# Kernel tuning notes

Hardware: AMD Instinct MI355X
Metric: run time of the kernel (lower is better)

The kernel has to match this reference:

```python
import jax, jax.numpy as jnp
import numpy as np

H, D = 16, 64  # head_num, head_dim
SCALE = 1.0 / D ** 0.5


def setup_inputs() -> dict:
    key = jax.random.key(0)
    ks = jax.random.split(key, 12)
    S, T, B, E = 2048, 2048, 2, 1024  # dec_seq, enc_seq, bs, input_dim
    return {
        "inputs": jax.random.normal(ks[0], (S, B, E), jnp.float32),
        "pos_embedding": jax.random.normal(ks[1], (T, 1, E), jnp.float32),
        "encoder_hidden_states": jax.random.normal(ks[2], (T, B, E), jnp.float32),
        "u": jax.random.normal(ks[3], (H, D), jnp.float32) * 0.02,
        "v": jax.random.normal(ks[4], (H, D), jnp.float32) * 0.02,
        "mask": jnp.zeros((S, T, 1), jnp.bool_),
        "Wkv": jax.random.normal(ks[5], (E, 2 * H * D), jnp.float32) * (E ** -0.5),
        "bkv": jnp.zeros((2 * H * D,), jnp.float32),
        "Wq": jax.random.normal(ks[6], (E, H * D), jnp.float32) * (E ** -0.5),
        "bq": jnp.zeros((H * D,), jnp.float32),
        "Wp": jax.random.normal(ks[7], (H * D, E), jnp.float32) * ((H * D) ** -0.5),
        "bp": jnp.zeros((E,), jnp.float32),
    }


def reference(inputs, pos_embedding, encoder_hidden_states, u, v, mask,
              Wkv, bkv, Wq, bq, Wp, bp):
    S, B, E = inputs.shape
    T = encoder_hidden_states.shape[0]
    # projections (fc_block == Linear)
    kv = encoder_hidden_states @ Wkv + bkv            # (T, B, 2HD)
    k, val = jnp.split(kv, 2, axis=-1)
    k = k.reshape(T, B, H, D)
    val = val.reshape(T, B, H, D)
    q = (inputs @ Wq + bq).reshape(S, B, H, D)
    q_u = q + u                                       # content bias (H, D) broadcast
    # content attention: (B, H, S, T)
    attn = jnp.einsum('sbhd,tbhd->bhst', q_u, k) * SCALE
    # mask (S, T, 1) -> (1, 1, S, T); all-False mask == original skip branch
    m = jnp.transpose(mask, (2, 0, 1))[:, None]
    attn = jnp.where(m, -jnp.inf, attn)
    attn = jax.nn.softmax(attn, axis=-1)
    # dropout is identity (eval)
    attn_vec = jnp.einsum('bhst,tbhd->sbhd', attn, val).reshape(S, B, H * D)
    return attn_vec @ Wp + bp                         # (S, B, E)
```

## Files before the change

### kernel.cpp

```cpp
#include <hip/hip_runtime.h>

#define Hh 16
#define Dd 64
#define Ss 2048
#define Tt 2048
#define Bb 2
#define Ee 1024
#define HD 1024
#define QSCALE 0.18033688011112042f

typedef __attribute__((ext_vector_type(8))) __bf16 bf16x8;
typedef __attribute__((ext_vector_type(4))) float f32x4;
typedef __attribute__((ext_vector_type(8))) unsigned short ushort8;

static __device__ __forceinline__ unsigned short f2b(float x) {
    union { float f; unsigned u; } v; v.f = x;
    unsigned r = v.u + 0x7FFFu + ((v.u >> 16) & 1u);
    return (unsigned short)(r >> 16);
}

static __device__ __forceinline__ unsigned cvtpk(float a, float b) {
    unsigned r;
    __asm__("v_cvt_pk_bf16_f32 %0, %1, %2" : "=v"(r) : "v"(a), "v"(b));
    return r;
}

static __device__ __forceinline__ void gld16(const unsigned short* g, unsigned short* l) {
    __builtin_amdgcn_global_load_lds(
        (const __attribute__((address_space(1))) unsigned int*)g,
        (__attribute__((address_space(3))) unsigned int*)l, 16, 0, 0);
}

__global__ __launch_bounds__(256) void prep(
    const float* __restrict__ enc, const float* __restrict__ inp,
    unsigned short* __restrict__ encb, unsigned short* __restrict__ inpb,
    const float* __restrict__ Wkv, const float* __restrict__ Wq, const float* __restrict__ Wp,
    unsigned short* __restrict__ Wkvt, unsigned short* __restrict__ Wqt,
    unsigned short* __restrict__ Wpt)
{
    __shared__ float tile[64][65];
    const int bx = blockIdx.x;
    const int tid = threadIdx.x;
    if (bx < 8192) {
        const int n4each = (Tt * Bb * Ee) / 4;
        int i = bx * 256 + tid;
        const float4* src; ushort4* dst; int j;
        if (i < n4each) { src = (const float4*)enc; dst = (ushort4*)encb; j = i; }
        else            { src = (const float4*)inp; dst = (ushort4*)inpb; j = i - n4each; }
        float4 v = src[j];
        ushort4 o; o.x = f2b(v.x); o.y = f2b(v.y); o.z = f2b(v.z); o.w = f2b(v.w);
        dst[j] = o;
        return;
    }
    int u = bx - 8192;
    const float* in; unsigned short* out; int C, cblk, rblk;
    if (u < 512)       { in = Wkv; out = Wkvt; C = 2048; cblk = u & 31; rblk = u >> 5; }
    else if (u < 768)  { int v = u - 512; in = Wq; out = Wqt; C = 1024; cblk = v & 15; rblk = v >> 4; }
    else               { int v = u - 768; in = Wp; out = Wpt; C = 1024; cblk = v & 15; rblk = v >> 4; }
    const int R = 1024;
    int c0 = cblk * 64, r0 = rblk * 64;
    int tx = tid & 63, ty = tid >> 6;
    for (int i = ty; i < 64; i += 4)
        tile[i][tx] = in[(r0 + i) * (long)C + c0 + tx];
    __syncthreads();
    int c_local = tid >> 2, g = tid & 3;
    ushort8 o0, o1;
#pragma unroll
    for (int k = 0; k < 8; k++) o0[k] = f2b(tile[g * 16 + k][c_local]);
#pragma unroll
    for (int k = 0; k < 8; k++) o1[k] = f2b(tile[g * 16 + 8 + k][c_local]);
    unsigned short* dst = &out[(c0 + c_local) * (long)R + r0 + g * 16];
    *(ushort8*)dst = o0;
    *(ushort8*)(dst + 8) = o1;
}

static __device__ __forceinline__ void gemm_core(
    const unsigned short* __restrict__ A, const unsigned short* __restrict__ Bt,
    int m0, int n0, unsigned short* lA, unsigned short* lB, f32x4 acc[4][4])
{
    const int tid = threadIdx.x;
    const int lane = tid & 63;
    const int wid = tid >> 6;
    const int waveM = (wid & 1) * 64, waveN = (wid >> 1) * 64;
    const int quad = lane >> 4, low = lane & 15;
#pragma unroll
    for (int i = 0; i < 4; i++)
#pragma unroll
        for (int j = 0; j < 4; j++) acc[i][j] = (f32x4)0.0f;

    for (int k0 = 0; k0 < 1024; k0 += 32) {
        __syncthreads();
        {
            int r0 = tid >> 2, s0 = tid & 3;
            int f1 = tid + 256, r1 = f1 >> 2, s1 = f1 & 3;
            gld16(&A[(m0 + r0) * 1024 + k0 + s0 * 8], &lA[tid * 8]);
            gld16(&A[(m0 + r1) * 1024 + k0 + s1 * 8], &lA[f1 * 8]);
            gld16(&Bt[(n0 + r0) * 1024 + k0 + s0 * 8], &lB[tid * 8]);
            gld16(&Bt[(n0 + r1) * 1024 + k0 + s1 * 8], &lB[f1 * 8]);
        }
        __syncthreads();
        bf16x8 af[4], bfr[4];
#pragma unroll
        for (int i = 0; i < 4; i++)
            af[i] = *(const bf16x8*)&lA[(waveM + i * 16 + low) * 32 + quad * 8];
#pragma unroll
        for (int j = 0; j < 4; j++)
            bfr[j] = *(const bf16x8*)&lB[(waveN + j * 16 + low) * 32 + quad * 8];
#pragma unroll
        for (int i = 0; i < 4; i++)
#pragma unroll
            for (int j = 0; j < 4; j++)
                acc[i][j] = __builtin_amdgcn_mfma_f32_16x16x32_bf16(af[i], bfr[j], acc[i][j], 0, 0, 0);
    }
}

__global__ __launch_bounds__(256) void gemm12(
    const unsigned short* __restrict__ encb, const unsigned short* __restrict__ Wkvt,
    const float* __restrict__ bkv,
    const unsigned short* __restrict__ inpb, const unsigned short* __restrict__ Wqt,
    const float* __restrict__ bq, const float* __restrict__ u,
    unsigned short* __restrict__ Kw, unsigned short* __restrict__ Vb,
    unsigned short* __restrict__ qw)
{
    __shared__ unsigned short smem[128 * 130];
    unsigned short* lA = smem;
    unsigned short* lB = smem + 128 * 32;
    const int bx = blockIdx.x;
    int z, m0, n0;
    const unsigned short *Ap, *Bp;
    if (bx < 512) { z = 0; m0 = (bx >> 4) * 128; n0 = (bx & 15) * 128; Ap = encb; Bp = Wkvt; }
    else { z = 1; int i = bx - 512; m0 = (i >> 3) * 128; n0 = (i & 7) * 128; Ap = inpb; Bp = Wqt; }
    f32x4 acc[4][4];
    gemm_core(Ap, Bp, m0, n0, lA, lB, acc);
    __syncthreads();

    const int lane = threadIdx.x & 63;
    const int wid = threadIdx.x >> 6;
    const int waveM = (wid & 1) * 64, waveN = (wid >> 1) * 64;
    const int quad = lane >> 4, low = lane & 15;
#pragma unroll
    for (int i = 0; i < 4; i++)
#pragma unroll
        for (int j = 0; j < 4; j++)
#pragma unroll
            for (int r = 0; r < 4; r++) {
                int lm = waveM + i * 16 + quad * 4 + r;
                int ln = waveN + j * 16 + low;
                int gn = n0 + ln;
                float val = acc[i][j][r];
                if (z == 0) val += bkv[gn];
                else        val = (val + bq[gn] + u[gn]) * QSCALE;
                smem[lm * 130 + ln] = f2b(val);
            }
    __syncthreads();

    const int tid = threadIdx.x;
    if (z == 0 && n0 >= 1024) {
        int d = tid & 63, hp = (tid >> 6) & 1, b = tid >> 7;
        int h = ((n0 - 1024) >> 6) + hp;
        int tb = m0 >> 7;
        unsigned short* dst = &Vb[((((b << 4) | h) * 32 + tb) * 64 + d) * 64];
#pragma unroll
        for (int c = 0; c < 8; c++) {
            ushort8 o;
#pragma unroll
            for (int k = 0; k < 8; k++)
                o[k] = smem[((c * 8 + k) * 2 + b) * 130 + hp * 64 + d];
            *(ushort8*)(dst + c * 8) = o;
        }
    } else {
        int gl = tid & 127, hp = tid >> 7;
        int gm = m0 + gl;
        int t = gm >> 1, b = gm & 1;
        int h = (n0 >> 6) + hp;
        unsigned short* base = (z == 0) ? Kw : qw;
        unsigned short* dst = &base[(((b << 4) | h) * 2048 + t) * 64];
        const unsigned short* src = &smem[gl * 130 + hp * 64];
#pragma unroll
        for (int c = 0; c < 8; c++) {
            ushort8 o;
#pragma unroll
            for (int k = 0; k < 8; k++) o[k] = src[c * 8 + k];
            *(ushort8*)(dst + c * 8) = o;
        }
    }
}

__global__ __launch_bounds__(256) void gemm3(
    const unsigned short* __restrict__ av, const unsigned short* __restrict__ Wpt,
    const float* __restrict__ bp, float* __restrict__ out)
{
    __shared__ unsigned short lA[128 * 32];
    __shared__ unsigned short lB[64 * 32];
    const int tid = threadIdx.x;
    const int lane = tid & 63;
    const int wid = tid >> 6;
    const int waveM = (wid & 1) * 64, waveN = (wid >> 1) * 32;
    const int m0 = blockIdx.y * 128, n0 = blockIdx.x * 64;
    const int quad = lane >> 4, low = lane & 15;

    f32x4 acc[4][2];
#pragma unroll
    for (int i = 0; i < 4; i++)
#pragma unroll
        for (int j = 0; j < 2; j++) acc[i][j] = (f32x4)0.0f;

    for (int k0 = 0; k0 < 1024; k0 += 32) {
        __syncthreads();
        {
            int r0 = tid >> 2, s0 = tid & 3;
            int f1 = tid + 256, r1 = f1 >> 2, s1 = f1 & 3;
            gld16(&av[(m0 + r0) * 1024 + k0 + s0 * 8], &lA[tid * 8]);
            gld16(&av[(m0 + r1) * 1024 + k0 + s1 * 8], &lA[f1 * 8]);
            gld16(&Wpt[(n0 + r0) * 1024 + k0 + s0 * 8], &lB[tid * 8]);
        }
        __syncthreads();
        bf16x8 af[4], bfr[2];
#pragma unroll
        for (int i = 0; i < 4; i++)
            af[i] = *(const bf16x8*)&lA[(waveM + i * 16 + low) * 32 + quad * 8];
#pragma unroll
        for (int j = 0; j < 2; j++)
            bfr[j] = *(const bf16x8*)&lB[(waveN + j * 16 + low) * 32 + quad * 8];
#pragma unroll
        for (int i = 0; i < 4; i++)
#pragma unroll
            for (int j = 0; j < 2; j++)
                acc[i][j] = __builtin_amdgcn_mfma_f32_16x16x32_bf16(af[i], bfr[j], acc[i][j], 0, 0, 0);
    }
#pragma unroll
    for (int i = 0; i < 4; i++)
#pragma unroll
        for (int j = 0; j < 2; j++)
#pragma unroll
            for (int r = 0; r < 4; r++) {
                int gm = m0 + waveM + i * 16 + quad * 4 + r;
                int gn = n0 + waveN + j * 16 + low;
                out[gm * 1024 + gn] = acc[i][j][r] + bp[gn];
            }
}

__global__ __launch_bounds__(256) void attn_kernel(
    const unsigned short* __restrict__ qw, const unsigned short* __restrict__ Kw,
    const unsigned short* __restrict__ Vb, unsigned short* __restrict__ av)
{
    __shared__ unsigned short kl[2][128 * 64];
    __shared__ unsigned short vt[2][64 * 64];
    __shared__ unsigned short pl[8][16 * 64];
    const int tid = threadIdx.x;
    const int lane = tid & 63;
    const int w = tid >> 6;
    const int quad = lane >> 4, low = lane & 15;
    const int swz = low & 7;
    const int bh = blockIdx.x & 31;
    const int s0 = (blockIdx.x >> 5) * 64;
    const int s_wave = s0 + w * 16;

    bf16x8 qf0, qf1;
    {
        const unsigned short* qa = &qw[(bh * 2048 + s_wave + low) * 64];
        qf0 = *(const bf16x8*)&qa[quad * 8];
        qf1 = *(const bf16x8*)&qa[32 + quad * 8];
    }
    bf16x8 ones;
    {
        ushort8 o1;
#pragma unroll
        for (int i = 0; i < 8; i++) o1[i] = 0x3F80;
        ones = *(bf16x8*)&o1;
    }
    f32x4 o[4];
    f32x4 l_acc = (f32x4)0.0f;
#pragma unroll
    for (int j = 0; j < 4; j++) o[j] = (f32x4)0.0f;

#pragma unroll
    for (int i = 0; i < 4; i++) {
        int fl = tid + i * 256;
        int row = fl >> 3, seg = fl & 7;
        gld16(&Kw[(bh * 2048 + row) * 64 + ((seg ^ (row & 7)) << 3)], &kl[0][fl * 8]);
    }
    __syncthreads();

    for (int t0 = 0; t0 < 2048; t0 += 128) {
        const int buf = (t0 >> 7) & 1;
#pragma unroll
        for (int i = 0; i < 4; i++) {
            int c2 = tid + i * 256;
            int win = c2 >> 9, inner = c2 & 511;
            int dd = inner >> 3, seg = inner & 7;
            gld16(&Vb[((bh * 32 + (t0 >> 6) + win) * 64 + dd) * 64 + ((seg ^ (dd & 7)) << 3)],
                  &vt[win][inner * 8]);
        }
        __builtin_amdgcn_sched_barrier(0);
        {
            int tn = (t0 + 128) & 2047;
#pragma unroll
            for (int i = 0; i < 4; i++) {
                int fl = tid + i * 256;
                int row = fl >> 3, seg = fl & 7;
                gld16(&Kw[(bh * 2048 + tn + row) * 64 + ((seg ^ (row & 7)) << 3)],
                      &kl[buf ^ 1][fl * 8]);
            }
        }
        __builtin_amdgcn_sched_barrier(0);

        f32x4 s0v[4], s1v[4];
#pragma unroll
        for (int jt = 0; jt < 4; jt++) {
            int r = jt * 16 + low;
            bf16x8 kb0 = *(const bf16x8*)&kl[buf][r * 64 + ((quad ^ swz) << 3)];
            bf16x8 kb1 = *(const bf16x8*)&kl[buf][r * 64 + (((quad ^ 4) ^ swz) << 3)];
            f32x4 a = (f32x4)0.0f;
            a = __builtin_amdgcn_mfma_f32_16x16x32_bf16(kb0, qf0, a, 0, 0, 0);
            s0v[jt] = __builtin_amdgcn_mfma_f32_16x16x32_bf16(kb1, qf1, a, 0, 0, 0);
        }
#pragma unroll
        for (int jt = 0; jt < 4; jt++)
#pragma unroll
            for (int r = 0; r < 4; r++)
                s0v[jt][r] = __builtin_amdgcn_exp2f(s0v[jt][r]);
#pragma unroll
        for (int jt = 0; jt < 4; jt++) {
            int c8 = jt * 2 + (quad >> 1), half = quad & 1;
            uint2 pk;
            pk.x = cvtpk(s0v[jt][0], s0v[jt][1]);
            pk.y = cvtpk(s0v[jt][2], s0v[jt][3]);
            *(uint2*)&pl[w * 2][low * 64 + ((c8 ^ swz) << 3) + half * 4] = pk;
        }

#pragma unroll
        for (int jt = 0; jt < 4; jt++) {
            int r = 64 + jt * 16 + low;
            bf16x8 kb0 = *(const bf16x8*)&kl[buf][r * 64 + ((quad ^ swz) << 3)];
            bf16x8 kb1 = *(const bf16x8*)&kl[buf][r * 64 + (((quad ^ 4) ^ swz) << 3)];
            f32x4 a = (f32x4)0.0f;
            a = __builtin_amdgcn_mfma_f32_16x16x32_bf16(kb0, qf0, a, 0, 0, 0);
            s1v[jt] = __builtin_amdgcn_mfma_f32_16x16x32_bf16(kb1, qf1, a, 0, 0, 0);
        }
#pragma unroll
        for (int jt = 0; jt < 4; jt++)
#pragma unroll
            for (int r = 0; r < 4; r++)
                s1v[jt][r] = __builtin_amdgcn_exp2f(s1v[jt][r]);
#pragma unroll
        for (int jt = 0; jt < 4; jt++) {
            int c8 = jt * 2 + (quad >> 1), half = quad & 1;
            uint2 pk;
            pk.x = cvtpk(s1v[jt][0], s1v[jt][1]);
            pk.y = cvtpk(s1v[jt][2], s1v[jt][3]);
            *(uint2*)&pl[w * 2 + 1][low * 64 + ((c8 ^ swz) << 3) + half * 4] = pk;
        }

        __asm__ volatile("s_waitcnt vmcnt(4)" ::: "memory");
        __builtin_amdgcn_s_barrier();
        __asm__ volatile("s_waitcnt lgkmcnt(0)" ::: "memory");
        __builtin_amdgcn_sched_barrier(0);

        bf16x8 pa0 = *(const bf16x8*)&pl[w * 2][low * 64 + ((quad ^ swz) << 3)];
        bf16x8 pa1 = *(const bf16x8*)&pl[w * 2][low * 64 + (((quad ^ 4) ^ swz) << 3)];
        l_acc = __builtin_amdgcn_mfma_f32_16x16x32_bf16(pa0, ones, l_acc, 0, 0, 0);
        l_acc = __builtin_amdgcn_mfma_f32_16x16x32_bf16(pa1, ones, l_acc, 0, 0, 0);
#pragma unroll
        for (int j = 0; j < 4; j++) {
            int dr = j * 16 + low;
            bf16x8 vb0 = *(const bf16x8*)&vt[0][dr * 64 + ((quad ^ swz) << 3)];
            bf16x8 vb1 = *(const bf16x8*)&vt[0][dr * 64 + (((quad ^ 4) ^ swz) << 3)];
            o[j] = __builtin_amdgcn_mfma_f32_16x16x32_bf16(pa0, vb0, o[j], 0, 0, 0);
            o[j] = __builtin_amdgcn_mfma_f32_16x16x32_bf16(pa1, vb1, o[j], 0, 0, 0);
        }
        bf16x8 pb0 = *(const bf16x8*)&pl[w * 2 + 1][low * 64 + ((quad ^ swz) << 3)];
        bf16x8 pb1 = *(const bf16x8*)&pl[w * 2 + 1][low * 64 + (((quad ^ 4) ^ swz) << 3)];
        l_acc = __builtin_amdgcn_mfma_f32_16x16x32_bf16(pb0, ones, l_acc, 0, 0, 0);
        l_acc = __builtin_amdgcn_mfma_f32_16x16x32_bf16(pb1, ones, l_acc, 0, 0, 0);
#pragma unroll
        for (int j = 0; j < 4; j++) {
            int dr = j * 16 + low;
            bf16x8 vb0 = *(const bf16x8*)&vt[1][dr * 64 + ((quad ^ swz) << 3)];
            bf16x8 vb1 = *(const bf16x8*)&vt[1][dr * 64 + (((quad ^ 4) ^ swz) << 3)];
            o[j] = __builtin_amdgcn_mfma_f32_16x16x32_bf16(pb0, vb0, o[j], 0, 0, 0);
            o[j] = __builtin_amdgcn_mfma_f32_16x16x32_bf16(pb1, vb1, o[j], 0, 0, 0);
        }

        __syncthreads();
    }

    int b = bh >> 4, hh = bh & 15;
#pragma unroll
    for (int j = 0; j < 4; j++) {
#pragma unroll
        for (int r = 0; r < 4; r++) {
            int sA_ = s_wave + quad * 4 + r;
            int d = j * 16 + low;
            av[(sA_ * 2 + b) * 1024 + hh * 64 + d] = f2b(o[j][r] / l_acc[r]);
        }
    }
}

extern "C" void kernel_launch(void* const* d_in, const int* in_sizes, int n_in,
                              void* d_out, int out_size, void* d_ws, size_t ws_size,
                              hipStream_t stream)
{
    const float* inputs = (const float*)d_in[0];
    const float* enc    = (const float*)d_in[2];
    const float* u      = (const float*)d_in[3];
    const float* Wkv    = (const float*)d_in[6];
    const float* bkv    = (const float*)d_in[7];
    const float* Wq     = (const float*)d_in[8];
    const float* bq     = (const float*)d_in[9];
    const float* Wp     = (const float*)d_in[10];
    const float* bp     = (const float*)d_in[11];
    float* out = (float*)d_out;

    char* ws = (char*)d_ws;
    unsigned short* enc_b = (unsigned short*)(ws + (0ull << 20));
    unsigned short* inp_b = (unsigned short*)(ws + (8ull << 20));
    unsigned short* Wkv_t = (unsigned short*)(ws + (16ull << 20));
    unsigned short* Wq_t  = (unsigned short*)(ws + (20ull << 20));
    unsigned short* Wp_t  = (unsigned short*)(ws + (22ull << 20));
    unsigned short* Kw    = (unsigned short*)(ws + (24ull << 20));
    unsigned short* Vb    = (unsigned short*)(ws + (32ull << 20));
    unsigned short* qw    = (unsigned short*)(ws + (40ull << 20));
    unsigned short* av    = (unsigned short*)(ws + (48ull << 20));

    prep<<<8192 + 1024, 256, 0, stream>>>(enc, inputs, enc_b, inp_b, Wkv, Wq, Wp,
                                          Wkv_t, Wq_t, Wp_t);
    gemm12<<<768, 256, 0, stream>>>(enc_b, Wkv_t, bkv, inp_b, Wq_t, bq, u, Kw, Vb, qw);
    attn_kernel<<<1024, 256, 0, stream>>>(qw, Kw, Vb, av);
    gemm3<<<dim3(16, 32), 256, 0, stream>>>(av, Wp_t, bp, out);
}
```

Measured before the change: 241.2 us.

## Rebuild P operand in registers via permlane swaps instead of LDS round-trip

The softmax probability tile was previously written to LDS and read back in the MFMA A-operand layout. It is now rearranged in registers with permlane32/permlane16 swaps, which removes the LDS store/load traffic, the per-wave P buffer and one lgkmcnt wait. The change also raises wave priority (s_setprio) around the MFMA sections so matrix work is favoured over the exp/convert phases. It depends on the permlane lane mapping exactly matching the old LDS transpose; a mismatch would give wrong results.

```diff
diff --git a/kernel.cpp b/kernel.cpp
--- a/kernel.cpp
+++ b/kernel.cpp
@@ -12,6 +12,7 @@
 typedef __attribute__((ext_vector_type(8))) __bf16 bf16x8;
 typedef __attribute__((ext_vector_type(4))) float f32x4;
 typedef __attribute__((ext_vector_type(8))) unsigned short ushort8;
+typedef __attribute__((ext_vector_type(2))) unsigned uint2v;
 
 static __device__ __forceinline__ unsigned short f2b(float x) {
     union { float f; unsigned u; } v; v.f = x;
@@ -29,6 +30,36 @@
     __builtin_amdgcn_global_load_lds(
         (const __attribute__((address_space(1))) unsigned int*)g,
         (__attribute__((address_space(3))) unsigned int*)l, 16, 0, 0);
+}
+
+static __device__ __forceinline__ void xquad(unsigned& a, unsigned& b) {
+    uint2v r1 = __builtin_amdgcn_permlane32_swap(a, b, false, false);
+    uint2v r2 = __builtin_amdgcn_permlane16_swap(r1[0], r1[1], false, false);
+    a = r2[0]; b = r2[1];
+}
+
+static __device__ __forceinline__ bf16x8 packp(unsigned w0, unsigned w1,
+                                               unsigned w2, unsigned w3) {
+    union { unsigned u[4]; bf16x8 v; } x;
+    x.u[0] = w0; x.u[1] = w1; x.u[2] = w2; x.u[3] = w3;
+    return x.v;
+}
+
+static __device__ __forceinline__ void mkP(f32x4 s[4], bf16x8& pa0, bf16x8& pa1) {
+#pragma unroll
+    for (int jt = 0; jt < 4; jt++)
+#pragma unroll
+        for (int r = 0; r < 4; r++) s[jt][r] = __builtin_amdgcn_exp2f(s[jt][r]);
+    unsigned a0 = cvtpk(s[0][0], s[0][1]), a1 = cvtpk(s[0][2], s[0][3]);
+    unsigned b0 = cvtpk(s[1][0], s[1][1]), b1 = cvtpk(s[1][2], s[1][3]);
+    unsigned c0 = cvtpk(s[2][0], s[2][1]), c1 = cvtpk(s[2][2], s[2][3]);
+    unsigned d0 = cvtpk(s[3][0], s[3][1]), d1 = cvtpk(s[3][2], s[3][3]);
+    xquad(a0, b0);
+    xquad(a1, b1);
+    xquad(c0, d0);
+    xquad(c1, d1);
+    pa0 = packp(a0, a1, b0, b1);
+    pa1 = packp(c0, c1, d0, d1);
 }
 
 __global__ __launch_bounds__(256) void prep(
@@ -246,7 +277,6 @@
 {
     __shared__ unsigned short kl[2][128 * 64];
     __shared__ unsigned short vt[2][64 * 64];
-    __shared__ unsigned short pl[8][16 * 64];
     const int tid = threadIdx.x;
     const int lane = tid & 63;
     const int w = tid >> 6;
@@ -306,6 +336,7 @@
         __builtin_amdgcn_sched_barrier(0);
 
         f32x4 s0v[4], s1v[4];
+        __builtin_amdgcn_s_setprio(1);
 #pragma unroll
         for (int jt = 0; jt < 4; jt++) {
             int r = jt * 16 + low;
@@ -315,20 +346,11 @@
             a = __builtin_amdgcn_mfma_f32_16x16x32_bf16(kb0, qf0, a, 0, 0, 0);
             s0v[jt] = __builtin_amdgcn_mfma_f32_16x16x32_bf16(kb1, qf1, a, 0, 0, 0);
         }
-#pragma unroll
-        for (int jt = 0; jt < 4; jt++)
-#pragma unroll
-            for (int r = 0; r < 4; r++)
-                s0v[jt][r] = __builtin_amdgcn_exp2f(s0v[jt][r]);
-#pragma unroll
-        for (int jt = 0; jt < 4; jt++) {
-            int c8 = jt * 2 + (quad >> 1), half = quad & 1;
-            uint2 pk;
-            pk.x = cvtpk(s0v[jt][0], s0v[jt][1]);
-            pk.y = cvtpk(s0v[jt][2], s0v[jt][3]);
-            *(uint2*)&pl[w * 2][low * 64 + ((c8 ^ swz) << 3) + half * 4] = pk;
-        }
-
+        __builtin_amdgcn_s_setprio(0);
+        bf16x8 p00, p01;
+        mkP(s0v, p00, p01);
+
+        __builtin_amdgcn_s_setprio(1);
 #pragma unroll
         for (int jt = 0; jt < 4; jt++) {
             int r = 64 + jt * 16 + low;
@@ -338,49 +360,36 @@
             a = __builtin_amdgcn_mfma_f32_16x16x32_bf16(kb0, qf0, a, 0, 0, 0);
             s1v[jt] = __builtin_amdgcn_mfma_f32_16x16x32_bf16(kb1, qf1, a, 0, 0, 0);
         }
-#pragma unroll
-        for (int jt = 0; jt < 4; jt++)
-#pragma unroll
-            for (int r = 0; r < 4; r++)
-                s1v[jt][r] = __builtin_amdgcn_exp2f(s1v[jt][r]);
-#pragma unroll
-        for (int jt = 0; jt < 4; jt++) {
-            int c8 = jt * 2 + (quad >> 1), half = quad & 1;
-            uint2 pk;
-            pk.x = cvtpk(s1v[jt][0], s1v[jt][1]);
-            pk.y = cvtpk(s1v[jt][2], s1v[jt][3]);
-            *(uint2*)&pl[w * 2 + 1][low * 64 + ((c8 ^ swz) << 3) + half * 4] = pk;
-        }
+        __builtin_amdgcn_s_setprio(0);
+        bf16x8 p10, p11;
+        mkP(s1v, p10, p11);
 
         __asm__ volatile("s_waitcnt vmcnt(4)" ::: "memory");
         __builtin_amdgcn_s_barrier();
-        __asm__ volatile("s_waitcnt lgkmcnt(0)" ::: "memory");
         __builtin_amdgcn_sched_barrier(0);
 
-        bf16x8 pa0 = *(const bf16x8*)&pl[w * 2][low * 64 + ((quad ^ swz) << 3)];
-        bf16x8 pa1 = *(const bf16x8*)&pl[w * 2][low * 64 + (((quad ^ 4) ^ swz) << 3)];
-        l_acc = __builtin_amdgcn_mfma_f32_16x16x32_bf16(pa0, ones, l_acc, 0, 0, 0);
-        l_acc = __builtin_amdgcn_mfma_f32_16x16x32_bf16(pa1, ones, l_acc, 0, 0, 0);
+        __builtin_amdgcn_s_setprio(1);
+        l_acc = __builtin_amdgcn_mfma_f32_16x16x32_bf16(p00, ones, l_acc, 0, 0, 0);
+        l_acc = __builtin_amdgcn_mfma_f32_16x16x32_bf16(p01, ones, l_acc, 0, 0, 0);
 #pragma unroll
         for (int j = 0; j < 4; j++) {
             int dr = j * 16 + low;
             bf16x8 vb0 = *(const bf16x8*)&vt[0][dr * 64 + ((quad ^ swz) << 3)];
             bf16x8 vb1 = *(const bf16x8*)&vt[0][dr * 64 + (((quad ^ 4) ^ swz) << 3)];
-            o[j] = __builtin_amdgcn_mfma_f32_16x16x32_bf16(pa0, vb0, o[j], 0, 0, 0);
-            o[j] = __builtin_amdgcn_mfma_f32_16x16x32_bf16(pa1, vb1, o[j], 0, 0, 0);
-        }
-        bf16x8 pb0 = *(const bf16x8*)&pl[w * 2 + 1][low * 64 + ((quad ^ swz) << 3)];
-        bf16x8 pb1 = *(const bf16x8*)&pl[w * 2 + 1][low * 64 + (((quad ^ 4) ^ swz) << 3)];
-        l_acc = __builtin_amdgcn_mfma_f32_16x16x32_bf16(pb0, ones, l_acc, 0, 0, 0);
-        l_acc = __builtin_amdgcn_mfma_f32_16x16x32_bf16(pb1, ones, l_acc, 0, 0, 0);
+            o[j] = __builtin_amdgcn_mfma_f32_16x16x32_bf16(p00, vb0, o[j], 0, 0, 0);
+            o[j] = __builtin_amdgcn_mfma_f32_16x16x32_bf16(p01, vb1, o[j], 0, 0, 0);
+        }
+        l_acc = __builtin_amdgcn_mfma_f32_16x16x32_bf16(p10, ones, l_acc, 0, 0, 0);
+        l_acc = __builtin_amdgcn_mfma_f32_16x16x32_bf16(p11, ones, l_acc, 0, 0, 0);
 #pragma unroll
         for (int j = 0; j < 4; j++) {
             int dr = j * 16 + low;
             bf16x8 vb0 = *(const bf16x8*)&vt[1][dr * 64 + ((quad ^ swz) << 3)];
             bf16x8 vb1 = *(const bf16x8*)&vt[1][dr * 64 + (((quad ^ 4) ^ swz) << 3)];
-            o[j] = __builtin_amdgcn_mfma_f32_16x16x32_bf16(pb0, vb0, o[j], 0, 0, 0);
-            o[j] = __builtin_amdgcn_mfma_f32_16x16x32_bf16(pb1, vb1, o[j], 0, 0, 0);
-        }
+            o[j] = __builtin_amdgcn_mfma_f32_16x16x32_bf16(p10, vb0, o[j], 0, 0, 0);
+            o[j] = __builtin_amdgcn_mfma_f32_16x16x32_bf16(p11, vb1, o[j], 0, 0, 0);
+        }
+        __builtin_amdgcn_s_setprio(0);
 
         __syncthreads();
     }
```

After: 239.5 us. About the same (-0.7%).
